# Performance work log

Hardware: AMD Instinct MI355X
Metric: run time of the kernel (lower is better)

Reference implementation:

```python
import jax, jax.numpy as jnp
import numpy as np

EMB, INT_EMB, BASIS = 128, 64, 8
NUM_RADIAL, NUM_SPHERICAL = 6, 7
E, T = 262144, 2097152
N_BEFORE, N_AFTER = 1, 2

silu = jax.nn.silu  # swish activation


def _glorot(key, shape):
    fan_in, fan_out = shape[0], shape[1]
    s = jnp.sqrt(2.0 / (fan_in + fan_out))
    return jax.random.normal(key, shape, dtype=jnp.float32) * s


def setup_inputs() -> dict:
    key = jax.random.key(0)
    ks = jax.random.split(key, 24)
    inp = {
        'm': jax.random.normal(ks[0], (E, EMB), dtype=jnp.float32),
        'rbf': jax.random.normal(ks[1], (E, NUM_RADIAL), dtype=jnp.float32),
        'sbf': jax.random.normal(ks[2], (T, NUM_RADIAL * NUM_SPHERICAL), dtype=jnp.float32),
        'src_idx': jax.random.randint(ks[3], (T,), 0, E, dtype=jnp.int32),
        'dst_idx': jax.random.randint(ks[4], (T,), 0, E, dtype=jnp.int32),
        # weights stored as [in, out] so forward is x @ W
        'W_rbf1': _glorot(ks[5], (NUM_RADIAL, BASIS)),
        'W_rbf2': _glorot(ks[6], (BASIS, EMB)),
        'W_sbf1': _glorot(ks[7], (NUM_RADIAL * NUM_SPHERICAL, BASIS)),
        'W_sbf2': _glorot(ks[8], (BASIS, INT_EMB)),
        'W_ji': _glorot(ks[9], (EMB, EMB)), 'b_ji': jnp.zeros((EMB,), jnp.float32),
        'W_kj': _glorot(ks[10], (EMB, EMB)), 'b_kj': jnp.zeros((EMB,), jnp.float32),
        'W_down': _glorot(ks[11], (EMB, INT_EMB)),
        'W_up': _glorot(ks[12], (INT_EMB, EMB)),
        'Wb1': jnp.stack([_glorot(jax.random.fold_in(ks[13], i), (EMB, EMB)) for i in range(N_BEFORE)]),
        'bb1': jnp.zeros((N_BEFORE, EMB), jnp.float32),
        'Wb2': jnp.stack([_glorot(jax.random.fold_in(ks[14], i), (EMB, EMB)) for i in range(N_BEFORE)]),
        'bb2': jnp.zeros((N_BEFORE, EMB), jnp.float32),
        'W_final': _glorot(ks[15], (EMB, EMB)), 'b_final': jnp.zeros((EMB,), jnp.float32),
        'Wa1': jnp.stack([_glorot(jax.random.fold_in(ks[16], i), (EMB, EMB)) for i in range(N_AFTER)]),
        'ba1': jnp.zeros((N_AFTER, EMB), jnp.float32),
        'Wa2': jnp.stack([_glorot(jax.random.fold_in(ks[17], i), (EMB, EMB)) for i in range(N_AFTER)]),
        'ba2': jnp.zeros((N_AFTER, EMB), jnp.float32),
    }
    return inp


def _residual(x, W1, b1, W2, b2):
    h = silu(x @ W1 + b1)
    h = silu(h @ W2 + b2)
    return x + h


def reference(m, rbf, sbf, src_idx, dst_idx,
              W_rbf1, W_rbf2, W_sbf1, W_sbf2,
              W_ji, b_ji, W_kj, b_kj, W_down, W_up,
              Wb1, bb1, Wb2, bb2, W_final, b_final,
              Wa1, ba1, Wa2, ba2):
    # edge_transfer
    rbf_e = (rbf @ W_rbf1) @ W_rbf2                 # [E, emb]
    x_ji = silu(m @ W_ji + b_ji)                    # [E, emb]
    x_kj = silu(m @ W_kj + b_kj)                    # [E, emb]
    x_kj = silu((x_kj * rbf_e) @ W_down)            # [E, int_emb]
    # msg_func over reversed line graph + sum aggregation
    sbf_t = (sbf @ W_sbf1) @ W_sbf2                 # [T, int_emb]
    msg = x_kj[src_idx] * sbf_t                     # [T, int_emb]
    m_update = jax.ops.segment_sum(msg, dst_idx, num_segments=E)  # [E, int_emb]
    m_update = silu(m_update @ W_up)                # [E, emb]
    m_update = m_update + x_ji
    for i in range(N_BEFORE):
        m_update = _residual(m_update, Wb1[i], bb1[i], Wb2[i], bb2[i])
    m_update = silu(m_update @ W_final + b_final)
    m_out = m + m_update
    for i in range(N_AFTER):
        m_out = _residual(m_out, Wa1[i], ba1[i], Wa2[i], ba2[i])
    return m_out
```

## Files before the change

### kernel.cpp

```cpp
#include <hip/hip_runtime.h>
#include <math.h>


#define E_N 262144
#define T_N 2097152
#define LDX 136

typedef __bf16 bf16_t;
typedef __attribute__((ext_vector_type(8))) __bf16 bf16x8;
typedef __attribute__((ext_vector_type(4))) float f32x4;

#define MFMA_B16(a, b, c) __builtin_amdgcn_mfma_f32_16x16x32_bf16(a, b, c, 0, 0, 0)

__device__ __forceinline__ float silu_f(float x) {
    return x / (1.0f + __expf(-x));
}

struct SwDesc { const float* src; bf16_t* dst; int Ksrc, KK, N, tbase; };
struct SwArgs { SwDesc d[12]; };

__global__ __launch_bounds__(256) void swizzle_kernel(SwArgs a, int total) {
    int t = blockIdx.x * 256 + threadIdx.x;
    if (t >= total) return;
    int i = 0;
#pragma unroll
    for (int j = 1; j < 12; j++) if (t >= a.d[j].tbase) i = j;
    SwDesc d = a.d[i];
    int lt = t - d.tbase;
    int lane = lt & 63, f = lt >> 6;
    int kk = f % d.KK, ct = f / d.KK;
    int q = lane >> 4, c = lane & 15, col = ct * 16 + c;
    bf16x8 v;
#pragma unroll
    for (int j = 0; j < 8; j++) {
        int k = kk * 32 + q * 8 + j;
        v[j] = (k < d.Ksrc) ? (bf16_t)d.src[(size_t)k * d.N + col] : (bf16_t)0.0f;
    }
    *(bf16x8*)(d.dst + (size_t)lt * 8) = v;
}

__global__ __launch_bounds__(256) void zero_kernel(float4* __restrict__ p, int n4) {
    int i = blockIdx.x * 256 + threadIdx.x;
    if (i < n4) p[i] = make_float4(0.f, 0.f, 0.f, 0.f);
}

template<int KK>
__device__ __forceinline__ void mfma_stage(const bf16_t* __restrict__ X,
                                           const bf16_t* __restrict__ Wsw,
                                           int lane, int ct0, f32x4 acc[4][2]) {
    const int q = lane >> 4, l15 = lane & 15;
    bf16x8 Bf[2][KK];
#pragma unroll
    for (int c = 0; c < 2; c++)
#pragma unroll
        for (int kk = 0; kk < KK; kk++)
            Bf[c][kk] = *(const bf16x8*)(Wsw + ((size_t)((ct0 + c) * KK + kk) * 64 + lane) * 8);
    f32x4 z = {0.f, 0.f, 0.f, 0.f};
#pragma unroll
    for (int rt = 0; rt < 4; rt++) { acc[rt][0] = z; acc[rt][1] = z; }
#pragma unroll
    for (int kk = 0; kk < KK; kk++) {
#pragma unroll
        for (int rt = 0; rt < 4; rt++) {
            bf16x8 a = *(const bf16x8*)(X + (rt * 16 + l15) * LDX + kk * 32 + q * 8);
            acc[rt][0] = MFMA_B16(a, Bf[0][kk], acc[rt][0]);
            acc[rt][1] = MFMA_B16(a, Bf[1][kk], acc[rt][1]);
        }
    }
}

__global__ __launch_bounds__(256, 3) void edge_kernel(
    const float* __restrict__ m, const float* __restrict__ rbf,
    const float* __restrict__ W_rbf1, const bf16_t* __restrict__ W_rbf2sw,
    const bf16_t* __restrict__ W_jisw, const float* __restrict__ b_ji,
    const bf16_t* __restrict__ W_kjsw, const float* __restrict__ b_kj,
    const bf16_t* __restrict__ W_downsw,
    bf16_t* __restrict__ x_ji_bf, float* __restrict__ x_kj) {
    __shared__ bf16_t Xm[64 * LDX];
    __shared__ bf16_t Xt[64 * LDX];
    __shared__ bf16_t hb[64 * 32];
    __shared__ float rl[64 * 6];
    const int tid = threadIdx.x;
    const int lane = tid & 63, wave = tid >> 6;
    const int q = lane >> 4, l15 = lane & 15;
    const int ct0 = wave * 2, wc0 = wave * 32;
    const int r0 = blockIdx.x * 64;

#pragma unroll
    for (int i = 0; i < 8; i++) {
        int e = (i * 256 + tid) * 4;
        int row = e >> 7, col = e & 127;
        float4 v = *(const float4*)(m + (size_t)(r0 + row) * 128 + col);
        bf16_t* d = Xm + row * LDX + col;
        d[0] = (bf16_t)v.x; d[1] = (bf16_t)v.y; d[2] = (bf16_t)v.z; d[3] = (bf16_t)v.w;
    }
    for (int i = tid; i < 64 * 6; i += 256) rl[i] = rbf[(size_t)r0 * 6 + i];
    for (int i = tid; i < 64 * 32; i += 256) hb[i] = (bf16_t)0.0f;
    __syncthreads();

    {
        int tt = tid >> 2, b0 = (tid & 3) << 1;
        float s0 = 0.f, s1 = 0.f;
#pragma unroll
        for (int k = 0; k < 6; k++) {
            float v = rl[tt * 6 + k];
            s0 = fmaf(v, W_rbf1[k * 8 + b0], s0);
            s1 = fmaf(v, W_rbf1[k * 8 + b0 + 1], s1);
        }
        hb[tt * 32 + b0] = (bf16_t)s0;
        hb[tt * 32 + b0 + 1] = (bf16_t)s1;
    }
    __syncthreads();

    f32x4 rbfe[4][2];
    {
        bf16x8 B0 = *(const bf16x8*)(W_rbf2sw + ((size_t)(ct0 + 0) * 64 + lane) * 8);
        bf16x8 B1 = *(const bf16x8*)(W_rbf2sw + ((size_t)(ct0 + 1) * 64 + lane) * 8);
        f32x4 z = {0.f, 0.f, 0.f, 0.f};
#pragma unroll
        for (int rt = 0; rt < 4; rt++) {
            bf16x8 a = *(const bf16x8*)(hb + (rt * 16 + l15) * 32 + q * 8);
            rbfe[rt][0] = MFMA_B16(a, B0, z);
            rbfe[rt][1] = MFMA_B16(a, B1, z);
        }
    }

    f32x4 acc[4][2];

    mfma_stage<4>(Xm, W_jisw, lane, ct0, acc);
    {
        float b0v = b_ji[wc0 + l15], b1v = b_ji[wc0 + 16 + l15];
#pragma unroll
        for (int rt = 0; rt < 4; rt++)
#pragma unroll
            for (int c = 0; c < 2; c++)
#pragma unroll
                for (int r = 0; r < 4; r++) {
                    int row = rt * 16 + q * 4 + r, col = wc0 + c * 16 + l15;
                    float v = silu_f(acc[rt][c][r] + (c ? b1v : b0v));
                    x_ji_bf[(size_t)(r0 + row) * 128 + col] = (bf16_t)v;
                }
    }

    mfma_stage<4>(Xm, W_kjsw, lane, ct0, acc);
    {
        float b0v = b_kj[wc0 + l15], b1v = b_kj[wc0 + 16 + l15];
#pragma unroll
        for (int rt = 0; rt < 4; rt++)
#pragma unroll
            for (int c = 0; c < 2; c++)
#pragma unroll
                for (int r = 0; r < 4; r++) {
                    int row = rt * 16 + q * 4 + r, col = wc0 + c * 16 + l15;
                    float v = silu_f(acc[rt][c][r] + (c ? b1v : b0v)) * rbfe[rt][c][r];
                    Xt[row * LDX + col] = (bf16_t)v;
                }
    }
    __syncthreads();

    {
        bf16x8 Bf[4];
#pragma unroll
        for (int kk = 0; kk < 4; kk++)
            Bf[kk] = *(const bf16x8*)(W_downsw + ((size_t)(wave * 4 + kk) * 64 + lane) * 8);
        f32x4 a2[4];
        f32x4 z = {0.f, 0.f, 0.f, 0.f};
#pragma unroll
        for (int rt = 0; rt < 4; rt++) a2[rt] = z;
#pragma unroll
        for (int kk = 0; kk < 4; kk++)
#pragma unroll
            for (int rt = 0; rt < 4; rt++) {
                bf16x8 a = *(const bf16x8*)(Xt + (rt * 16 + l15) * LDX + kk * 32 + q * 8);
                a2[rt] = MFMA_B16(a, Bf[kk], a2[rt]);
            }
#pragma unroll
        for (int rt = 0; rt < 4; rt++)
#pragma unroll
            for (int r = 0; r < 4; r++) {
                int row = rt * 16 + q * 4 + r, col = wave * 16 + l15;
                x_kj[(size_t)(r0 + row) * 64 + col] = silu_f(a2[rt][r]);
            }
    }
}

__global__ __launch_bounds__(256, 4) void triplet_kernel(
    const float* __restrict__ sbf, const int* __restrict__ src_idx,
    const int* __restrict__ dst_idx,
    const float* __restrict__ W_sbf1, const float* __restrict__ W_sbf2,
    const float* __restrict__ x_kj, float* __restrict__ m_update) {
    __shared__ float S[64 * 42];
    __shared__ float B[64 * 8];
    __shared__ float W1l[42 * 8];
    const int tid = threadIdx.x;
    const int t0 = blockIdx.x * 64;

    {
        const float4* s4 = (const float4*)(sbf + (size_t)t0 * 42);
        float4* d4 = (float4*)S;
        for (int i = tid; i < 672; i += 256) d4[i] = s4[i];
    }
    for (int i = tid; i < 336; i += 256) W1l[i] = W_sbf1[i];
    __syncthreads();

    {
        int tt = tid >> 2, b0 = (tid & 3) << 1;
        float s0 = 0.f, s1 = 0.f;
#pragma unroll
        for (int k = 0; k < 42; k++) {
            float v = S[tt * 42 + k];
            s0 = fmaf(v, W1l[k * 8 + b0], s0);
            s1 = fmaf(v, W1l[k * 8 + b0 + 1], s1);
        }
        B[tt * 8 + b0] = s0;
        B[tt * 8 + b0 + 1] = s1;
    }
    __syncthreads();

    const int wave = tid >> 6, lane = tid & 63;
    float w2[8];
#pragma unroll
    for (int k = 0; k < 8; k++) w2[k] = W_sbf2[k * 64 + lane];
    const int base_tt = wave * 16;
#pragma unroll 4
    for (int u = 0; u < 16; u++) {
        int tt = base_tt + u;
        int t = t0 + tt;
        int se = src_idx[t];
        int de = dst_idx[t];
        float acc = 0.f;
#pragma unroll
        for (int k = 0; k < 8; k++) acc = fmaf(B[tt * 8 + k], w2[k], acc);
        float xk = x_kj[(size_t)se * 64 + lane];
        atomicAdd(&m_update[(size_t)de * 64 + lane], xk * acc);
    }
}

__global__ __launch_bounds__(256, 3) void post_kernel(
    const float* __restrict__ m, const bf16_t* __restrict__ x_ji_bf,
    const float* __restrict__ m_up,
    const bf16_t* __restrict__ W_upsw,
    const bf16_t* __restrict__ Wb1sw, const float* __restrict__ bb1,
    const bf16_t* __restrict__ Wb2sw, const float* __restrict__ bb2,
    const bf16_t* __restrict__ Wfinsw, const float* __restrict__ b_final,
    const bf16_t* __restrict__ Wa1s0, const bf16_t* __restrict__ Wa1s1,
    const float* __restrict__ ba1,
    const bf16_t* __restrict__ Wa2s0, const bf16_t* __restrict__ Wa2s1,
    const float* __restrict__ ba2,
    float* __restrict__ out) {
    __shared__ bf16_t X0[64 * LDX];
    __shared__ bf16_t X1[64 * LDX];
    const int tid = threadIdx.x;
    const int lane = tid & 63, wave = tid >> 6;
    const int q = lane >> 4, l15 = lane & 15;
    const int ct0 = wave * 2, wc0 = wave * 32;
    const int r0 = blockIdx.x * 64;

#pragma unroll
    for (int i = 0; i < 4; i++) {
        int e = (i * 256 + tid) * 4;
        int row = e >> 6, col = e & 63;
        float4 v = *(const float4*)(m_up + (size_t)(r0 + row) * 64 + col);
        bf16_t* d = X0 + row * LDX + col;
        d[0] = (bf16_t)v.x; d[1] = (bf16_t)v.y; d[2] = (bf16_t)v.z; d[3] = (bf16_t)v.w;
    }
    __syncthreads();

    f32x4 acc[4][2];
    float res[4][2][4];

    mfma_stage<2>(X0, W_upsw, lane, ct0, acc);
#pragma unroll
    for (int rt = 0; rt < 4; rt++)
#pragma unroll
        for (int c = 0; c < 2; c++)
#pragma unroll
            for (int r = 0; r < 4; r++) {
                int row = rt * 16 + q * 4 + r, col = wc0 + c * 16 + l15;
                float v = silu_f(acc[rt][c][r]) + (float)x_ji_bf[(size_t)(r0 + row) * 128 + col];
                res[rt][c][r] = v;
                X1[row * LDX + col] = (bf16_t)v;
            }
    __syncthreads();

    mfma_stage<4>(X1, Wb1sw, lane, ct0, acc);
    {
        float b0v = bb1[wc0 + l15], b1v = bb1[wc0 + 16 + l15];
#pragma unroll
        for (int rt = 0; rt < 4; rt++)
#pragma unroll
            for (int c = 0; c < 2; c++)
#pragma unroll
                for (int r = 0; r < 4; r++) {
                    int row = rt * 16 + q * 4 + r, col = wc0 + c * 16 + l15;
                    X0[row * LDX + col] = (bf16_t)silu_f(acc[rt][c][r] + (c ? b1v : b0v));
                }
    }
    __syncthreads();

    mfma_stage<4>(X0, Wb2sw, lane, ct0, acc);
    {
        float b0v = bb2[wc0 + l15], b1v = bb2[wc0 + 16 + l15];
#pragma unroll
        for (int rt = 0; rt < 4; rt++)
#pragma unroll
            for (int c = 0; c < 2; c++)
#pragma unroll
                for (int r = 0; r < 4; r++) {
                    int row = rt * 16 + q * 4 + r, col = wc0 + c * 16 + l15;
                    float v = res[rt][c][r] + silu_f(acc[rt][c][r] + (c ? b1v : b0v));
                    res[rt][c][r] = v;
                    X1[row * LDX + col] = (bf16_t)v;
                }
    }
    __syncthreads();

    mfma_stage<4>(X1, Wfinsw, lane, ct0, acc);
    {
        float b0v = b_final[wc0 + l15], b1v = b_final[wc0 + 16 + l15];
#pragma unroll
        for (int rt = 0; rt < 4; rt++)
#pragma unroll
            for (int c = 0; c < 2; c++)
#pragma unroll
                for (int r = 0; r < 4; r++) {
                    int row = rt * 16 + q * 4 + r, col = wc0 + c * 16 + l15;
                    float v = silu_f(acc[rt][c][r] + (c ? b1v : b0v))
                              + m[(size_t)(r0 + row) * 128 + col];
                    res[rt][c][r] = v;
                    X0[row * LDX + col] = (bf16_t)v;
                }
    }
    __syncthreads();

    mfma_stage<4>(X0, Wa1s0, lane, ct0, acc);
    {
        float b0v = ba1[wc0 + l15], b1v = ba1[wc0 + 16 + l15];
#pragma unroll
        for (int rt = 0; rt < 4; rt++)
#pragma unroll
            for (int c = 0; c < 2; c++)
#pragma unroll
                for (int r = 0; r < 4; r++) {
                    int row = rt * 16 + q * 4 + r, col = wc0 + c * 16 + l15;
                    X1[row * LDX + col] = (bf16_t)silu_f(acc[rt][c][r] + (c ? b1v : b0v));
                }
    }
    __syncthreads();

    mfma_stage<4>(X1, Wa2s0, lane, ct0, acc);
    {
        float b0v = ba2[wc0 + l15], b1v = ba2[wc0 + 16 + l15];
#pragma unroll
        for (int rt = 0; rt < 4; rt++)
#pragma unroll
            for (int c = 0; c < 2; c++)
#pragma unroll
                for (int r = 0; r < 4; r++) {
                    int row = rt * 16 + q * 4 + r, col = wc0 + c * 16 + l15;
                    float v = res[rt][c][r] + silu_f(acc[rt][c][r] + (c ? b1v : b0v));
                    res[rt][c][r] = v;
                    X0[row * LDX + col] = (bf16_t)v;
                }
    }
    __syncthreads();

    mfma_stage<4>(X0, Wa1s1, lane, ct0, acc);
    {
        float b0v = ba1[128 + wc0 + l15], b1v = ba1[128 + wc0 + 16 + l15];
#pragma unroll
        for (int rt = 0; rt < 4; rt++)
#pragma unroll
            for (int c = 0; c < 2; c++)
#pragma unroll
                for (int r = 0; r < 4; r++) {
                    int row = rt * 16 + q * 4 + r, col = wc0 + c * 16 + l15;
                    X1[row * LDX + col] = (bf16_t)silu_f(acc[rt][c][r] + (c ? b1v : b0v));
                }
    }
    __syncthreads();

    mfma_stage<4>(X1, Wa2s1, lane, ct0, acc);
    {
        float b0v = ba2[128 + wc0 + l15], b1v = ba2[128 + wc0 + 16 + l15];
#pragma unroll
        for (int rt = 0; rt < 4; rt++)
#pragma unroll
            for (int c = 0; c < 2; c++)
#pragma unroll
                for (int r = 0; r < 4; r++) {
                    int row = rt * 16 + q * 4 + r, col = wc0 + c * 16 + l15;
                    out[(size_t)(r0 + row) * 128 + col]
                        = res[rt][c][r] + silu_f(acc[rt][c][r] + (c ? b1v : b0v));
                }
    }
}

extern "C" void kernel_launch(void* const* d_in, const int* in_sizes, int n_in,
                              void* d_out, int out_size, void* d_ws, size_t ws_size,
                              hipStream_t stream) {
    const float* m      = (const float*)d_in[0];
    const float* rbf    = (const float*)d_in[1];
    const float* sbf    = (const float*)d_in[2];
    const int*   src    = (const int*)d_in[3];
    const int*   dst    = (const int*)d_in[4];
    const float* W_rbf1 = (const float*)d_in[5];
    const float* W_rbf2 = (const float*)d_in[6];
    const float* W_sbf1 = (const float*)d_in[7];
    const float* W_sbf2 = (const float*)d_in[8];
    const float* W_ji   = (const float*)d_in[9];
    const float* b_ji   = (const float*)d_in[10];
    const float* W_kj   = (const float*)d_in[11];
    const float* b_kj   = (const float*)d_in[12];
    const float* W_down = (const float*)d_in[13];
    const float* W_up   = (const float*)d_in[14];
    const float* Wb1    = (const float*)d_in[15];
    const float* bb1    = (const float*)d_in[16];
    const float* Wb2    = (const float*)d_in[17];
    const float* bb2    = (const float*)d_in[18];
    const float* W_final= (const float*)d_in[19];
    const float* b_final= (const float*)d_in[20];
    const float* Wa1    = (const float*)d_in[21];
    const float* ba1    = (const float*)d_in[22];
    const float* Wa2    = (const float*)d_in[23];
    const float* ba2    = (const float*)d_in[24];
    float* out = (float*)d_out;

    size_t off_xkj = (size_t)E_N * 128 * sizeof(bf16_t);
    size_t off_mup = off_xkj + (size_t)E_N * 64 * sizeof(float);
    size_t off_w   = off_mup + (size_t)E_N * 64 * sizeof(float);
    size_t w_elems = 167936;
    if (ws_size < off_w + w_elems * sizeof(bf16_t)) return;

    bf16_t* x_ji_bf = (bf16_t*)d_ws;
    float*  x_kj    = (float*)((char*)d_ws + off_xkj);
    float*  m_upd   = (float*)((char*)d_ws + off_mup);
    bf16_t* wts     = (bf16_t*)((char*)d_ws + off_w);

    bf16_t* W_rbf2sw = wts;
    bf16_t* W_jisw   = wts + 4096;
    bf16_t* W_kjsw   = wts + 20480;
    bf16_t* W_downsw = wts + 36864;
    bf16_t* W_upsw   = wts + 45056;
    bf16_t* Wb1sw    = wts + 53248;
    bf16_t* Wb2sw    = wts + 69632;
    bf16_t* Wfinsw   = wts + 86016;
    bf16_t* Wa1sw0   = wts + 102400;
    bf16_t* Wa1sw1   = wts + 118784;
    bf16_t* Wa2sw0   = wts + 135168;
    bf16_t* Wa2sw1   = wts + 151552;

    SwArgs sa;
    int tb = 0;
    auto set = [&](int i, const float* s, bf16_t* d, int Ksrc, int KK, int N) {
        sa.d[i] = SwDesc{s, d, Ksrc, KK, N, tb};
        tb += (N / 16) * KK * 64;
    };
    set(0,  W_rbf2,        W_rbf2sw, 8,   1, 128);
    set(1,  W_ji,          W_jisw,   128, 4, 128);
    set(2,  W_kj,          W_kjsw,   128, 4, 128);
    set(3,  W_down,        W_downsw, 128, 4, 64);
    set(4,  W_up,          W_upsw,   64,  2, 128);
    set(5,  Wb1,           Wb1sw,    128, 4, 128);
    set(6,  Wb2,           Wb2sw,    128, 4, 128);
    set(7,  W_final,       Wfinsw,   128, 4, 128);
    set(8,  Wa1,           Wa1sw0,   128, 4, 128);
    set(9,  Wa1 + 16384,   Wa1sw1,   128, 4, 128);
    set(10, Wa2,           Wa2sw0,   128, 4, 128);
    set(11, Wa2 + 16384,   Wa2sw1,   128, 4, 128);
    int total = tb;

    swizzle_kernel<<<(total + 255) / 256, 256, 0, stream>>>(sa, total);

    zero_kernel<<<(E_N * 64 / 4) / 256, 256, 0, stream>>>((float4*)m_upd, E_N * 64 / 4);

    edge_kernel<<<E_N / 64, 256, 0, stream>>>(m, rbf, W_rbf1, W_rbf2sw,
                                              W_jisw, b_ji, W_kjsw, b_kj, W_downsw,
                                              x_ji_bf, x_kj);

    triplet_kernel<<<T_N / 64, 256, 0, stream>>>(sbf, src, dst, W_sbf1, W_sbf2,
                                                 x_kj, m_upd);

    post_kernel<<<E_N / 64, 256, 0, stream>>>(m, x_ji_bf, m_upd, W_upsw,
                                              Wb1sw, bb1, Wb2sw, bb2,
                                              Wfinsw, b_final,
                                              Wa1sw0, Wa1sw1, ba1,
                                              Wa2sw0, Wa2sw1, ba2, out);
}
```

Measured before the change: 1.240 ms.

## Replace atomic scatter with CSR sort-by-destination and per-edge gather reduction

The triplet scatter with float atomics is replaced by a counting sort on dst_idx: a histogram kernel (which also computes the sbf basis projection and stores it as bf16), a three-pass prefix scan, and a fill kernel that builds a permutation. A gather kernel then has one wave per edge sum its triplets in registers and write m_update once as bf16. This removes 2M×64 global atomics and the zeroing of the fp32 m_update, at the cost of several extra launches, a random-atomic fill pass, serial per-edge loops with dependent index loads, and bf16 rounding of intermediates.

Result: slower. 1.432 ms (+15.5%).

```diff
diff --git a/kernel.cpp b/kernel.cpp
--- a/kernel.cpp
+++ b/kernel.cpp
@@ -184,61 +184,128 @@
     }
 }
 
-__global__ __launch_bounds__(256, 4) void triplet_kernel(
-    const float* __restrict__ sbf, const int* __restrict__ src_idx,
-    const int* __restrict__ dst_idx,
-    const float* __restrict__ W_sbf1, const float* __restrict__ W_sbf2,
-    const float* __restrict__ x_kj, float* __restrict__ m_update) {
+
+__global__ __launch_bounds__(256) void histB_kernel(
+    const float* __restrict__ sbf, const int* __restrict__ dst_idx,
+    const float* __restrict__ W_sbf1,
+    bf16_t* __restrict__ Bg, int* __restrict__ counts) {
     __shared__ float S[64 * 42];
-    __shared__ float B[64 * 8];
-    __shared__ float W1l[42 * 8];
+    __shared__ float W1l[336];
     const int tid = threadIdx.x;
     const int t0 = blockIdx.x * 64;
-
     {
         const float4* s4 = (const float4*)(sbf + (size_t)t0 * 42);
         float4* d4 = (float4*)S;
         for (int i = tid; i < 672; i += 256) d4[i] = s4[i];
     }
     for (int i = tid; i < 336; i += 256) W1l[i] = W_sbf1[i];
-    __syncthreads();
-
-    {
-        int tt = tid >> 2, b0 = (tid & 3) << 1;
-        float s0 = 0.f, s1 = 0.f;
-#pragma unroll
-        for (int k = 0; k < 42; k++) {
-            float v = S[tt * 42 + k];
-            s0 = fmaf(v, W1l[k * 8 + b0], s0);
-            s1 = fmaf(v, W1l[k * 8 + b0 + 1], s1);
-        }
-        B[tt * 8 + b0] = s0;
-        B[tt * 8 + b0 + 1] = s1;
-    }
-    __syncthreads();
-
+    if (tid < 64) atomicAdd(&counts[dst_idx[t0 + tid]], 1);
+    __syncthreads();
+
+    int tt = tid >> 2, b0 = (tid & 3) << 1;
+    float s0 = 0.f, s1 = 0.f;
+#pragma unroll
+    for (int k = 0; k < 42; k++) {
+        float v = S[tt * 42 + k];
+        s0 = fmaf(v, W1l[k * 8 + b0], s0);
+        s1 = fmaf(v, W1l[k * 8 + b0 + 1], s1);
+    }
+    Bg[(size_t)(t0 + tt) * 8 + b0]     = (bf16_t)s0;
+    Bg[(size_t)(t0 + tt) * 8 + b0 + 1] = (bf16_t)s1;
+}
+
+__global__ __launch_bounds__(256) void scan1_kernel(
+    const int4* __restrict__ c4, int* __restrict__ offs, int* __restrict__ bsums) {
+    __shared__ int sc[256];
+    const int tid = threadIdx.x;
+    int idx = blockIdx.x * 256 + tid;
+    int4 c = c4[idx];
+    int s = c.x + c.y + c.z + c.w;
+    sc[tid] = s;
+    __syncthreads();
+#pragma unroll
+    for (int d = 1; d < 256; d <<= 1) {
+        int t = (tid >= d) ? sc[tid - d] : 0;
+        __syncthreads();
+        sc[tid] += t;
+        __syncthreads();
+    }
+    int excl = sc[tid] - s;
+    int4 o;
+    o.x = excl; o.y = excl + c.x; o.z = o.y + c.y; o.w = o.z + c.z;
+    ((int4*)offs)[idx] = o;
+    if (tid == 255) bsums[blockIdx.x] = sc[255];
+}
+
+__global__ __launch_bounds__(256) void scan2_kernel(
+    const int* __restrict__ bsums, int* __restrict__ bsums2) {
+    __shared__ int sc[256];
+    const int tid = threadIdx.x;
+    int v = bsums[tid];
+    sc[tid] = v;
+    __syncthreads();
+#pragma unroll
+    for (int d = 1; d < 256; d <<= 1) {
+        int t = (tid >= d) ? sc[tid - d] : 0;
+        __syncthreads();
+        sc[tid] += t;
+        __syncthreads();
+    }
+    bsums2[tid] = sc[tid] - v;
+}
+
+__global__ __launch_bounds__(256) void scan3_kernel(
+    int* __restrict__ offs, const int* __restrict__ bsums2, int* __restrict__ cursor) {
+    int i = blockIdx.x * 256 + threadIdx.x;
+    int o = offs[i] + bsums2[i >> 10];
+    offs[i] = o;
+    cursor[i] = o;
+}
+
+__global__ __launch_bounds__(256) void fill_kernel(
+    const int* __restrict__ dst_idx, int* __restrict__ cursor, int* __restrict__ perm) {
+    int t = blockIdx.x * 256 + threadIdx.x;
+    int d = dst_idx[t];
+    int pos = atomicAdd(&cursor[d], 1);
+    perm[pos] = t;
+}
+
+__global__ __launch_bounds__(256) void gather_kernel(
+    const int* __restrict__ offs, const int* __restrict__ counts,
+    const int* __restrict__ perm, const int* __restrict__ src_idx,
+    const bf16_t* __restrict__ Bg, const float* __restrict__ W_sbf2,
+    const float* __restrict__ x_kj, bf16_t* __restrict__ m_upd) {
+    __shared__ float w2s[512];
+    const int tid = threadIdx.x;
+    w2s[tid] = W_sbf2[tid];
+    w2s[tid + 256] = W_sbf2[tid + 256];
+    __syncthreads();
     const int wave = tid >> 6, lane = tid & 63;
-    float w2[8];
-#pragma unroll
-    for (int k = 0; k < 8; k++) w2[k] = W_sbf2[k * 64 + lane];
-    const int base_tt = wave * 16;
-#pragma unroll 4
-    for (int u = 0; u < 16; u++) {
-        int tt = base_tt + u;
-        int t = t0 + tt;
+    const int e = blockIdx.x * 4 + wave;
+    const int start = offs[e];
+    const int cnt = counts[e];
+    float w2r[8];
+#pragma unroll
+    for (int k = 0; k < 8; k++) w2r[k] = w2s[k * 64 + lane];
+    float acc = 0.f;
+    int t = (cnt > 0) ? perm[start] : 0;
+    for (int i = 0; i < cnt; i++) {
+        int tn = (i + 1 < cnt) ? perm[start + i + 1] : 0;
         int se = src_idx[t];
-        int de = dst_idx[t];
-        float acc = 0.f;
-#pragma unroll
-        for (int k = 0; k < 8; k++) acc = fmaf(B[tt * 8 + k], w2[k], acc);
-        float xk = x_kj[(size_t)se * 64 + lane];
-        atomicAdd(&m_update[(size_t)de * 64 + lane], xk * acc);
-    }
+        bf16x8 bv = *(const bf16x8*)(Bg + (size_t)t * 8);
+        float xv = x_kj[(size_t)se * 64 + lane];
+        float s = 0.f;
+#pragma unroll
+        for (int k = 0; k < 8; k++) s = fmaf((float)bv[k], w2r[k], s);
+        acc = fmaf(xv, s, acc);
+        t = tn;
+    }
+    m_upd[(size_t)e * 64 + lane] = (bf16_t)acc;
 }
 
 __global__ __launch_bounds__(256, 3) void post_kernel(
     const float* __restrict__ m, const bf16_t* __restrict__ x_ji_bf,
-    const float* __restrict__ m_up,
+    const bf16_t* __restrict__ m_up,
     const bf16_t* __restrict__ W_upsw,
     const bf16_t* __restrict__ Wb1sw, const float* __restrict__ bb1,
     const bf16_t* __restrict__ Wb2sw, const float* __restrict__ bb2,
@@ -257,12 +324,11 @@
     const int r0 = blockIdx.x * 64;
 
 #pragma unroll
-    for (int i = 0; i < 4; i++) {
-        int e = (i * 256 + tid) * 4;
-        int row = e >> 6, col = e & 63;
-        float4 v = *(const float4*)(m_up + (size_t)(r0 + row) * 64 + col);
-        bf16_t* d = X0 + row * LDX + col;
-        d[0] = (bf16_t)v.x; d[1] = (bf16_t)v.y; d[2] = (bf16_t)v.z; d[3] = (bf16_t)v.w;
+    for (int i = 0; i < 2; i++) {
+        int idx = i * 256 + tid;
+        int row = idx >> 3, col = (idx & 7) * 8;
+        *(bf16x8*)(X0 + row * LDX + col) =
+            *(const bf16x8*)(m_up + (size_t)(r0 + row) * 64 + col);
     }
     __syncthreads();
 
@@ -426,15 +492,28 @@
     const float* ba2    = (const float*)d_in[24];
     float* out = (float*)d_out;
 
-    size_t off_xkj = (size_t)E_N * 128 * sizeof(bf16_t);
-    size_t off_mup = off_xkj + (size_t)E_N * 64 * sizeof(float);
-    size_t off_w   = off_mup + (size_t)E_N * 64 * sizeof(float);
+    size_t off_xkj  = (size_t)E_N * 128 * sizeof(bf16_t);
+    size_t off_mup  = off_xkj  + (size_t)E_N * 64 * sizeof(float);
+    size_t off_B    = off_mup  + (size_t)E_N * 64 * sizeof(bf16_t);
+    size_t off_perm = off_B    + (size_t)T_N * 8 * sizeof(bf16_t);
+    size_t off_cnt  = off_perm + (size_t)T_N * sizeof(int);
+    size_t off_offs = off_cnt  + (size_t)E_N * sizeof(int);
+    size_t off_cur  = off_offs + (size_t)E_N * sizeof(int);
+    size_t off_bs   = off_cur  + (size_t)E_N * sizeof(int);
+    size_t off_w    = off_bs   + 4096;
     size_t w_elems = 167936;
     if (ws_size < off_w + w_elems * sizeof(bf16_t)) return;
 
     bf16_t* x_ji_bf = (bf16_t*)d_ws;
     float*  x_kj    = (float*)((char*)d_ws + off_xkj);
-    float*  m_upd   = (float*)((char*)d_ws + off_mup);
+    bf16_t* m_upd   = (bf16_t*)((char*)d_ws + off_mup);
+    bf16_t* Bg      = (bf16_t*)((char*)d_ws + off_B);
+    int*    perm    = (int*)((char*)d_ws + off_perm);
+    int*    counts  = (int*)((char*)d_ws + off_cnt);
+    int*    offs    = (int*)((char*)d_ws + off_offs);
+    int*    cursor  = (int*)((char*)d_ws + off_cur);
+    int*    bsums   = (int*)((char*)d_ws + off_bs);
+    int*    bsums2  = bsums + 256;
     bf16_t* wts     = (bf16_t*)((char*)d_ws + off_w);
 
     bf16_t* W_rbf2sw = wts;
@@ -472,14 +551,20 @@
 
     swizzle_kernel<<<(total + 255) / 256, 256, 0, stream>>>(sa, total);
 
-    zero_kernel<<<(E_N * 64 / 4) / 256, 256, 0, stream>>>((float4*)m_upd, E_N * 64 / 4);
+    zero_kernel<<<256, 256, 0, stream>>>((float4*)counts, E_N / 4);
+
+    histB_kernel<<<T_N / 64, 256, 0, stream>>>(sbf, dst, W_sbf1, Bg, counts);
+    scan1_kernel<<<E_N / 1024, 256, 0, stream>>>((const int4*)counts, offs, bsums);
+    scan2_kernel<<<1, 256, 0, stream>>>(bsums, bsums2);
+    scan3_kernel<<<E_N / 256, 256, 0, stream>>>(offs, bsums2, cursor);
+    fill_kernel<<<T_N / 256, 256, 0, stream>>>(dst, cursor, perm);
 
     edge_kernel<<<E_N / 64, 256, 0, stream>>>(m, rbf, W_rbf1, W_rbf2sw,
                                               W_jisw, b_ji, W_kjsw, b_kj, W_downsw,
                                               x_ji_bf, x_kj);
 
-    triplet_kernel<<<T_N / 64, 256, 0, stream>>>(sbf, src, dst, W_sbf1, W_sbf2,
-                                                 x_kj, m_upd);
+    gather_kernel<<<E_N / 4, 256, 0, stream>>>(offs, counts, perm, src,
+                                               Bg, W_sbf2, x_kj, m_upd);
 
     post_kernel<<<E_N / 64, 256, 0, stream>>>(m, x_ji_bf, m_upd, W_upsw,
                                               Wb1sw, bb1, Wb2sw, bb2,
```
